# Kernel optimization log

Measured on AMD Instinct MI355X. Metric: run time of the kernel, lower is better.

## Reference

```python
import jax, jax.numpy as jnp
import numpy as np

E = 1024      # embedding_size
K = 64        # key_size
D = 64        # head_size
S = 1024      # context_size
V = 32000     # vocab_size
H = 16        # layer_size (heads per layer)
L = 8         # num_layers
B = 2


def _pe():
    pos = jnp.arange(S, dtype=jnp.float32)[:, None]
    i = jnp.arange(E, dtype=jnp.float32)[None, :]
    ang = pos / jnp.power(10000.0, 2.0 * i / E)
    return jnp.where((jnp.arange(E) % 2 == 0)[None, :], jnp.sin(ang), jnp.cos(ang))


def setup_inputs() -> dict:
    key = jax.random.key(0)
    ks = iter(jax.random.split(key, 32))
    s = 0.02
    n = lambda shape: jax.random.normal(next(ks), shape, dtype=jnp.float32) * s
    inp = {
        "tokens": jax.random.randint(next(ks), (B, S), 0, V),
        "emb": n((V, E)),
        "pe": _pe(),
        "k1w": n((L, H, K, E)), "k1b": n((L, H, K)),
        "k2w": n((L, H, K, K)), "k2b": n((L, H, K)),
        "q1w": n((L, H, K, E)), "q1b": n((L, H, K)),
        "q2w": n((L, H, K, K)), "q2b": n((L, H, K)),
        "vw": n((L, H, D, E)), "vb": n((L, H, D)),
        "lnw": jnp.ones((L, E), jnp.float32), "lnb": jnp.zeros((L, E), jnp.float32),
        "p1w": n((L, E, E)), "p1b": n((L, E)),
        "p2w": n((L, E, E)), "p2b": n((L, E)),
        "predw": n((V, E)), "predb": n((V,)),
    }
    return inp


def reference(tokens, emb, pe, k1w, k1b, k2w, k2b, q1w, q1b, q2w, q2b,
              vw, vb, lnw, lnb, p1w, p1b, p2w, p2b, predw, predb):
    relu = jax.nn.relu
    x = emb[tokens] + pe[:tokens.shape[1]]                       # [B,S,E]
    seq = tokens.shape[1]
    # Faithful to original: tril (past+diag) gets the -1e10 penalty.
    mask = jnp.tril(jnp.ones((seq, seq), x.dtype)) * -1e10
    for l in range(L):
        # two-layer ReLU MLPs for K and Q, batched over heads
        k = relu(jnp.einsum('bse,hke->bhsk', x, k1w[l]) + k1b[l][None, :, None, :])
        k = relu(jnp.einsum('bhsk,hjk->bhsj', k, k2w[l]) + k2b[l][None, :, None, :])
        q = relu(jnp.einsum('bse,hke->bhsk', x, q1w[l]) + q1b[l][None, :, None, :])
        q = relu(jnp.einsum('bhsk,hjk->bhsj', q, q2w[l]) + q2b[l][None, :, None, :])
        v = jnp.einsum('bse,hde->bhsd', x, vw[l]) + vb[l][None, :, None, :]
        scores = jnp.einsum('bhsk,bhtk->bhst', q, k) / (K ** 0.5) + mask
        w = jax.nn.softmax(scores, axis=-1)
        o = jnp.einsum('bhst,bhtd->bhsd', w, v)                  # [B,H,S,D]
        o = o.transpose(0, 2, 1, 3).reshape(x.shape[0], seq, H * D)
        y = x + o
        mu = y.mean(-1, keepdims=True)
        var = ((y - mu) ** 2).mean(-1, keepdims=True)
        yn = (y - mu) / jnp.sqrt(var + 1e-5) * lnw[l] + lnb[l]
        h1 = relu(yn @ p1w[l].T + p1b[l])
        x = relu(h1 @ p2w[l].T + p2b[l])
    logits = x @ predw.T + predb                                 # [B,S,V]
    return logits
```

## Files before the change

### kernel.cpp

```cpp
#include <hip/hip_runtime.h>


typedef __attribute__((ext_vector_type(8))) short bf16x8;
typedef __attribute__((ext_vector_type(4))) float f32x4;

#define L_ 8
#define S_ 1024
#define E_ 1024
#define B_ 2
#define H_ 16
#define V_ 32000
#define M_ 2048

__device__ __forceinline__ unsigned short f2b(float f) {
  union { float f; unsigned int u; } v; v.f = f;
  unsigned int r = v.u + 0x7FFFu + ((v.u >> 16) & 1u);
  return (unsigned short)(r >> 16);
}

#define GLDS16(gptr, lptr)                                                            \
  __builtin_amdgcn_global_load_lds(                                                   \
      (const __attribute__((address_space(1))) unsigned int*)(gptr),                  \
      (__attribute__((address_space(3))) unsigned int*)(lptr), 16, 0, 0)

__global__ void cvt_kernel(const float* __restrict__ src, unsigned short* __restrict__ dst) {
  size_t i = ((size_t)blockIdx.x * 256 + threadIdx.x) * 4;
  float4 v = *(const float4*)(src + i);
  unsigned short* d = dst + i;
  d[0] = f2b(v.x); d[1] = f2b(v.y); d[2] = f2b(v.z); d[3] = f2b(v.w);
}

__global__ void cvt_seg_kernel(const float* __restrict__ src, unsigned short* __restrict__ dst,
                               int perLayer, int dstStride, int dstOff) {
  size_t i = ((size_t)blockIdx.x * 256 + threadIdx.x) * 4;
  int l = (int)(i / perLayer);
  int off = (int)(i - (size_t)l * perLayer);
  float4 v = *(const float4*)(src + i);
  unsigned short* d = dst + (size_t)l * dstStride + dstOff + off;
  d[0] = f2b(v.x); d[1] = f2b(v.y); d[2] = f2b(v.z); d[3] = f2b(v.w);
}

__global__ void biascat_kernel(const float* __restrict__ k1b, const float* __restrict__ q1b,
                               const float* __restrict__ vb, float* __restrict__ bcat) {
  int i = blockIdx.x * 256 + threadIdx.x;
  int l = i / 3072, j = i - l * 3072;
  float v;
  if (j < 1024)      v = k1b[l * 1024 + j];
  else if (j < 2048) v = q1b[l * 1024 + j - 1024];
  else               v = vb [l * 1024 + j - 2048];
  bcat[i] = v;
}

__global__ void embed_kernel(const int* __restrict__ tokens, const float* __restrict__ emb,
                             const float* __restrict__ pe, float* __restrict__ x32,
                             unsigned short* __restrict__ xb) {
  int row = blockIdx.x;
  int s = row & (S_ - 1);
  int e0 = threadIdx.x * 4;
  int tok = tokens[row];
  float4 ev = *(const float4*)(emb + (size_t)tok * E_ + e0);
  float4 pv = *(const float4*)(pe + (size_t)s * E_ + e0);
  float4 v; v.x = ev.x + pv.x; v.y = ev.y + pv.y; v.z = ev.z + pv.z; v.w = ev.w + pv.w;
  *(float4*)(x32 + (size_t)row * E_ + e0) = v;
  ushort4 o; o.x = f2b(v.x); o.y = f2b(v.y); o.z = f2b(v.z); o.w = f2b(v.w);
  *(ushort4*)(xb + (size_t)row * E_ + e0) = o;
}

template <int BM, int BN, int RELU, int OBF, int OF32, int VT>
__global__ __launch_bounds__(256) void gemm97(
    const unsigned short* __restrict__ A, const unsigned short* __restrict__ W,
    const float* __restrict__ bias, unsigned short* __restrict__ Cb,
    float* __restrict__ Cf, unsigned short* __restrict__ vTp,
    int K, int N, int reluN) {
  constexpr int AR = BM / 64;
  constexpr int BR = BN / 64;
  constexpr int FM = BM / 32;
  constexpr int FN = BN / 32;
  __shared__ __align__(16) unsigned short sA[BM * 32];
  __shared__ __align__(16) unsigned short sB[BN * 32];
  const int tid = threadIdx.x;
  const int lane = tid & 63, wave = tid >> 6;
  const int l16 = lane & 15, lhi = lane >> 4;

  const int gx = gridDim.x, nwg = gx * gridDim.y;
  int o = blockIdx.y * gx + blockIdx.x;
  int wg = ((nwg & 7) == 0) ? ((o & 7) * (nwg >> 3) + (o >> 3)) : o;
  const int row0 = (wg % gx) * BM, col0 = (wg / gx) * BN;

  const int wm = (wave >> 1) * (BM / 2), wn = (wave & 1) * (BN / 2);

  const int srow = wave * 16 + (lane >> 2);
  const int scol = ((lane & 3) ^ ((lane >> 3) & 3)) * 8;
  const int cx = (lhi ^ ((l16 >> 1) & 3)) * 8;

  f32x4 acc[FM][FN] = {};

  for (int k0 = 0; k0 < K; k0 += 32) {
#pragma unroll
    for (int r = 0; r < AR; r++)
      GLDS16(A + (size_t)(row0 + r * 64 + srow) * K + k0 + scol,
             sA + r * 2048 + wave * 512);
#pragma unroll
    for (int r = 0; r < BR; r++)
      GLDS16(W + (size_t)(col0 + r * 64 + srow) * K + k0 + scol,
             sB + r * 2048 + wave * 512);
    __syncthreads();

    bf16x8 af[FM], bf[FN];
#pragma unroll
    for (int i = 0; i < FM; i++)
      af[i] = *(const bf16x8*)(sA + (wm + i * 16 + l16) * 32 + cx);
#pragma unroll
    for (int j = 0; j < FN; j++)
      bf[j] = *(const bf16x8*)(sB + (wn + j * 16 + l16) * 32 + cx);
#pragma unroll
    for (int i = 0; i < FM; i++)
#pragma unroll
      for (int j = 0; j < FN; j++)
        acc[i][j] = __builtin_amdgcn_mfma_f32_16x16x32_bf16(bf[j], af[i], acc[i][j], 0, 0, 0);
    __syncthreads();
  }

#pragma unroll
  for (int j = 0; j < FN; j++) {
    const int colb = col0 + wn + j * 16 + lhi * 4;
    const float4 bv = *(const float4*)(bias + colb);
    const bool dorelu = (RELU == 1) || (RELU == 2 && colb < reluN);
#pragma unroll
    for (int i = 0; i < FM; i++) {
      const int row = row0 + wm + i * 16 + l16;
      float v0 = acc[i][j][0] + bv.x, v1 = acc[i][j][1] + bv.y;
      float v2 = acc[i][j][2] + bv.z, v3 = acc[i][j][3] + bv.w;
      if (dorelu) {
        v0 = fmaxf(v0, 0.f); v1 = fmaxf(v1, 0.f);
        v2 = fmaxf(v2, 0.f); v3 = fmaxf(v3, 0.f);
      }
      if (OBF) {
        ushort4 ob; ob.x = f2b(v0); ob.y = f2b(v1); ob.z = f2b(v2); ob.w = f2b(v3);
        *(ushort4*)(Cb + (size_t)row * N + colb) = ob;
      }
      if (OF32) {
        float4 of; of.x = v0; of.y = v1; of.z = v2; of.w = v3;
        *(float4*)(Cf + (size_t)row * N + colb) = of;
      }
      if (VT) {
        if (colb - lhi * 4 >= 2048) {
          const int hd0 = colb - 2048;
          const int bq = row >> 10, s = row & 1023;
          unsigned short* vr = vTp + ((size_t)(bq << 10) + hd0) * 1024 + s;
          vr[0] = f2b(v0); vr[1024] = f2b(v1); vr[2048] = f2b(v2); vr[3072] = f2b(v3);
        }
      }
    }
  }
}

__global__ __launch_bounds__(512, 2) void gemm256(
    const unsigned short* __restrict__ A, const unsigned short* __restrict__ W,
    const float* __restrict__ bias, float* __restrict__ Cf) {
  constexpr int KK = 1024;
  constexpr int NT = 32;
  __shared__ __align__(16) unsigned short sA[3][8192];
  __shared__ __align__(16) unsigned short sB[3][8192];
  const int tid = threadIdx.x;
  const int lane = tid & 63, wave = tid >> 6;
  const int l16 = lane & 15, lhi = lane >> 4;
  const int wr = wave >> 2, wc = wave & 3;

  const int o = blockIdx.x;
  const int wg = (o & 7) * 125 + (o >> 3);
  const int row0 = (wg & 7) * 256;
  const int col0 = (wg >> 3) * 256;

  const int pr0 = tid >> 2;
  const int xc = ((tid & 3) ^ ((pr0 >> 1) & 3)) * 8;
  const int ldsx = (lhi ^ ((l16 >> 1) & 3)) * 8;

  f32x4 acc[8][4] = {};

  auto stage = [&](int kt) {
    const int slot = kt % 3;
    const int k0 = kt * 32;
#pragma unroll
    for (int is = 0; is < 2; is++) {
      GLDS16(A + (size_t)(row0 + is * 128 + pr0) * KK + k0 + xc,
             &sA[slot][(is * 512 + (tid & ~63)) * 8]);
      GLDS16(W + (size_t)(col0 + is * 128 + pr0) * KK + k0 + xc,
             &sB[slot][(is * 512 + (tid & ~63)) * 8]);
    }
  };

  stage(0);
  stage(1);

  for (int kt = 0; kt < NT; kt++) {
    const int slot = kt % 3;
    if (kt == NT - 1) { asm volatile("s_waitcnt vmcnt(0)" ::: "memory"); }
    else              { asm volatile("s_waitcnt vmcnt(4)" ::: "memory"); }
    __builtin_amdgcn_s_barrier();
    __builtin_amdgcn_sched_barrier(0);

    const unsigned short* sa = &sA[slot][(wr * 128) * 32];
    const unsigned short* sb = &sB[slot][(wc * 64) * 32];
    bf16x8 bf[4];
#pragma unroll
    for (int j = 0; j < 4; j++)
      bf[j] = *(const bf16x8*)(sb + (j * 16 + l16) * 32 + ldsx);

#pragma unroll
    for (int ip = 0; ip < 4; ip++) {
      bf16x8 af0 = *(const bf16x8*)(sa + ((ip * 2) * 16 + l16) * 32 + ldsx);
      bf16x8 af1 = *(const bf16x8*)(sa + ((ip * 2 + 1) * 16 + l16) * 32 + ldsx);
      if (ip == 0 && kt + 2 < NT) stage(kt + 2);
      __builtin_amdgcn_s_setprio(1);
#pragma unroll
      for (int j = 0; j < 4; j++)
        acc[ip * 2][j] = __builtin_amdgcn_mfma_f32_16x16x32_bf16(bf[j], af0, acc[ip * 2][j], 0, 0, 0);
#pragma unroll
      for (int j = 0; j < 4; j++)
        acc[ip * 2 + 1][j] = __builtin_amdgcn_mfma_f32_16x16x32_bf16(bf[j], af1, acc[ip * 2 + 1][j], 0, 0, 0);
      __builtin_amdgcn_s_setprio(0);
    }
  }

#pragma unroll
  for (int j = 0; j < 4; j++) {
    const int colb = col0 + wc * 64 + j * 16 + lhi * 4;
    const float4 bv = *(const float4*)(bias + colb);
#pragma unroll
    for (int i = 0; i < 8; i++) {
      const int row = row0 + wr * 128 + i * 16 + l16;
      float4 of;
      of.x = acc[i][j][0] + bv.x; of.y = acc[i][j][1] + bv.y;
      of.z = acc[i][j][2] + bv.z; of.w = acc[i][j][3] + bv.w;
      *(float4*)(Cf + (size_t)row * V_ + colb) = of;
    }
  }
}

__global__ __launch_bounds__(256) void k2q2_kernel(
    const unsigned short* __restrict__ kqv, const unsigned short* __restrict__ wk2,
    const unsigned short* __restrict__ wq2, const float* __restrict__ k2b,
    const float* __restrict__ q2b, unsigned short* __restrict__ kbuf,
    unsigned short* __restrict__ qbuf) {
  const int m0 = blockIdx.x * 64;
  const int h = blockIdx.y;
  const int which = blockIdx.z;
  const unsigned short* Ap = kqv + (which ? 1024 : 0) + h * 64;
  const unsigned short* Wp = (which ? wq2 : wk2) + h * 4096;
  const float* bias = (which ? q2b : k2b) + h * 64;
  unsigned short* out = (which ? qbuf : kbuf) + h * 64;
  const int lane = threadIdx.x & 63, wave = threadIdx.x >> 6;
  const int l16 = lane & 15, lhi = lane >> 4;
  const int mw = m0 + wave * 16;

  f32x4 acc[4] = {};
#pragma unroll
  for (int ks = 0; ks < 2; ks++) {
    bf16x8 a = *(const bf16x8*)(Ap + (size_t)(mw + l16) * 3072 + ks * 32 + (lhi << 3));
#pragma unroll
    for (int j = 0; j < 4; j++) {
      bf16x8 b = *(const bf16x8*)(Wp + (j * 16 + l16) * 64 + ks * 32 + (lhi << 3));
      acc[j] = __builtin_amdgcn_mfma_f32_16x16x32_bf16(a, b, acc[j], 0, 0, 0);
    }
  }
#pragma unroll
  for (int j = 0; j < 4; j++) {
    float bv = bias[j * 16 + l16];
#pragma unroll
    for (int r = 0; r < 4; r++) {
      int row = mw + (lhi << 2) + r;
      float v = fmaxf(acc[j][r] + bv, 0.f);
      out[(size_t)row * 1024 + j * 16 + l16] = f2b(v);
    }
  }
}

__global__ __launch_bounds__(128) void attn_kernel(
    const unsigned short* __restrict__ qbuf,
    const unsigned short* __restrict__ kbuf,
    const unsigned short* __restrict__ vT,
    float* __restrict__ o32) {
  constexpr int LD = 72;
  __shared__ __align__(16) unsigned short sP[2 * 16 * LD];
  const int bid = blockIdx.x;
  const int bh = bid & 31, qt = bid >> 5;
  const int b = bh >> 4, h = bh & 15;
  const int tid = threadIdx.x, lane = tid & 63, w = tid >> 6;
  const int l16 = lane & 15, lhi = lane >> 4;
  const int base = b * S_;
  const int qrow = qt * 32 + w * 16 + l16;

  bf16x8 aq[2];
#pragma unroll
  for (int ks = 0; ks < 2; ks++)
    aq[ks] = *(const bf16x8*)(qbuf + (size_t)(base + qrow) * 1024 + h * 64 + ks * 32 + (lhi << 3));

  f32x4 oacc[4] = {};
  float mrun[4], lrun[4];
#pragma unroll
  for (int r = 0; r < 4; r++) { mrun[r] = -1e10f; lrun[r] = 0.f; }
  const int srow = qt * 32 + w * 16 + (lhi << 2);
  const int t0s = (qt == 31) ? 0 : ((qt >> 1) << 6);

  unsigned short* sPw = sP + w * 16 * LD;

  for (int t0 = t0s; t0 < S_; t0 += 64) {
    f32x4 sacc[4] = {};
#pragma unroll
    for (int ks = 0; ks < 2; ks++) {
#pragma unroll
      for (int nt = 0; nt < 4; nt++) {
        bf16x8 bk = *(const bf16x8*)(kbuf + (size_t)(base + t0 + nt * 16 + l16) * 1024 +
                                     h * 64 + ks * 32 + (lhi << 3));
        sacc[nt] = __builtin_amdgcn_mfma_f32_16x16x32_bf16(aq[ks], bk, sacc[nt], 0, 0, 0);
      }
    }
    float p[4][4];
#pragma unroll
    for (int nt = 0; nt < 4; nt++) {
      int tcol = t0 + nt * 16 + l16;
#pragma unroll
      for (int r = 0; r < 4; r++) {
        float v = sacc[nt][r] * 0.125f;
        if (tcol <= srow + r) v = -1e10f;
        p[nt][r] = v;
      }
    }
#pragma unroll
    for (int r = 0; r < 4; r++) {
      float m = fmaxf(fmaxf(p[0][r], p[1][r]), fmaxf(p[2][r], p[3][r]));
#pragma unroll
      for (int off = 1; off < 16; off <<= 1) m = fmaxf(m, __shfl_xor(m, off, 16));
      float mnew = fmaxf(mrun[r], m);
      float alpha = __expf(mrun[r] - mnew);
      mrun[r] = mnew;
      float rs = 0.f;
#pragma unroll
      for (int nt = 0; nt < 4; nt++) {
        float e = __expf(p[nt][r] - mnew);
        p[nt][r] = e; rs += e;
      }
#pragma unroll
      for (int off = 1; off < 16; off <<= 1) rs += __shfl_xor(rs, off, 16);
      lrun[r] = lrun[r] * alpha + rs;
      oacc[0][r] *= alpha; oacc[1][r] *= alpha; oacc[2][r] *= alpha; oacc[3][r] *= alpha;
    }
#pragma unroll
    for (int nt = 0; nt < 4; nt++)
#pragma unroll
      for (int r = 0; r < 4; r++)
        sPw[((lhi << 2) + r) * LD + nt * 16 + l16] = f2b(p[nt][r]);
#pragma unroll
    for (int ks = 0; ks < 2; ks++) {
      bf16x8 ap = *(const bf16x8*)(sPw + l16 * LD + ks * 32 + (lhi << 3));
#pragma unroll
      for (int nt = 0; nt < 4; nt++) {
        bf16x8 bv = *(const bf16x8*)(vT + (size_t)(bh * 64 + nt * 16 + l16) * 1024 +
                                     t0 + ks * 32 + (lhi << 3));
        oacc[nt] = __builtin_amdgcn_mfma_f32_16x16x32_bf16(ap, bv, oacc[nt], 0, 0, 0);
      }
    }
  }
#pragma unroll
  for (int nt = 0; nt < 4; nt++) {
#pragma unroll
    for (int r = 0; r < 4; r++) {
      int row = srow + r;
      o32[(size_t)(base + row) * 1024 + h * 64 + nt * 16 + l16] = oacc[nt][r] / lrun[r];
    }
  }
}

__global__ __launch_bounds__(256) void ln_kernel(
    const float* __restrict__ x32, const float* __restrict__ o32,
    const float* __restrict__ lnw, const float* __restrict__ lnb,
    unsigned short* __restrict__ yn) {
  __shared__ float red[8];
  const int row = blockIdx.x, tid = threadIdx.x;
  const int lane = tid & 63, wave = tid >> 6;
  const int e0 = tid * 4;
  float4 xv = *(const float4*)(x32 + (size_t)row * E_ + e0);
  float4 ov = *(const float4*)(o32 + (size_t)row * E_ + e0);
  float y0 = xv.x + ov.x, y1 = xv.y + ov.y, y2 = xv.z + ov.z, y3 = xv.w + ov.w;
  float s = y0 + y1 + y2 + y3;
  float sq = y0 * y0 + y1 * y1 + y2 * y2 + y3 * y3;
#pragma unroll
  for (int off = 32; off > 0; off >>= 1) {
    s += __shfl_xor(s, off, 64);
    sq += __shfl_xor(sq, off, 64);
  }
  if (lane == 0) { red[wave * 2] = s; red[wave * 2 + 1] = sq; }
  __syncthreads();
  float ts = red[0] + red[2] + red[4] + red[6];
  float tsq = red[1] + red[3] + red[5] + red[7];
  float mu = ts * (1.f / E_);
  float var = tsq * (1.f / E_) - mu * mu;
  float rstd = rsqrtf(var + 1e-5f);
  float4 gv = *(const float4*)(lnw + e0);
  float4 bv = *(const float4*)(lnb + e0);
  ushort4 o;
  o.x = f2b((y0 - mu) * rstd * gv.x + bv.x);
  o.y = f2b((y1 - mu) * rstd * gv.y + bv.y);
  o.z = f2b((y2 - mu) * rstd * gv.z + bv.z);
  o.w = f2b((y3 - mu) * rstd * gv.w + bv.w);
  *(ushort4*)(yn + (size_t)row * E_ + e0) = o;
}

extern "C" void kernel_launch(void* const* d_in, const int* in_sizes, int n_in,
                              void* d_out, int out_size, void* d_ws, size_t ws_size,
                              hipStream_t stream) {
  const int* tokens  = (const int*)d_in[0];
  const float* emb   = (const float*)d_in[1];
  const float* pe    = (const float*)d_in[2];
  const float* k1w   = (const float*)d_in[3];
  const float* k1b   = (const float*)d_in[4];
  const float* k2w   = (const float*)d_in[5];
  const float* k2b   = (const float*)d_in[6];
  const float* q1w   = (const float*)d_in[7];
  const float* q1b   = (const float*)d_in[8];
  const float* q2w   = (const float*)d_in[9];
  const float* q2b   = (const float*)d_in[10];
  const float* vw    = (const float*)d_in[11];
  const float* vb    = (const float*)d_in[12];
  const float* lnw   = (const float*)d_in[13];
  const float* lnb   = (const float*)d_in[14];
  const float* p1w   = (const float*)d_in[15];
  const float* p1b   = (const float*)d_in[16];
  const float* p2w   = (const float*)d_in[17];
  const float* p2b   = (const float*)d_in[18];
  const float* predw = (const float*)d_in[19];
  const float* predb = (const float*)d_in[20];
  float* out = (float*)d_out;

  char* p = (char*)d_ws;
  auto alloc = [&](size_t bytes) -> char* {
    char* r = p; p += (bytes + 255) & ~(size_t)255; return r;
  };
  unsigned short* wcat  = (unsigned short*)alloc((size_t)L_ * 3072 * 1024 * 2);
  unsigned short* wk2   = (unsigned short*)alloc((size_t)L_ * H_ * 64 * 64 * 2);
  unsigned short* wq2   = (unsigned short*)alloc((size_t)L_ * H_ * 64 * 64 * 2);
  unsigned short* wp1   = (unsigned short*)alloc((size_t)L_ * 1024 * 1024 * 2);
  unsigned short* wp2   = (unsigned short*)alloc((size_t)L_ * 1024 * 1024 * 2);
  unsigned short* wpred = (unsigned short*)alloc((size_t)V_ * 1024 * 2);
  float*          bcat  = (float*)alloc((size_t)L_ * 3072 * 4);
  float*          x32   = (float*)alloc((size_t)M_ * 1024 * 4);
  unsigned short* xb    = (unsigned short*)alloc((size_t)M_ * 1024 * 2);
  unsigned short* kqv   = (unsigned short*)alloc((size_t)M_ * 3072 * 2);
  unsigned short* kbuf  = (unsigned short*)alloc((size_t)M_ * 1024 * 2);
  unsigned short* qbuf  = (unsigned short*)alloc((size_t)M_ * 1024 * 2);
  unsigned short* vTb   = (unsigned short*)alloc((size_t)32 * 64 * 1024 * 2);
  float*          o32   = (float*)alloc((size_t)M_ * 1024 * 4);
  unsigned short* yn    = (unsigned short*)alloc((size_t)M_ * 1024 * 2);
  unsigned short* h1    = (unsigned short*)alloc((size_t)M_ * 1024 * 2);
  if ((size_t)(p - (char*)d_ws) > ws_size) return;

  cvt_seg_kernel<<<8192, 256, 0, stream>>>(k1w, wcat, 1048576, 3145728, 0);
  cvt_seg_kernel<<<8192, 256, 0, stream>>>(q1w, wcat, 1048576, 3145728, 1048576);
  cvt_seg_kernel<<<8192, 256, 0, stream>>>(vw,  wcat, 1048576, 3145728, 2097152);
  cvt_kernel<<<512, 256, 0, stream>>>(k2w, wk2);
  cvt_kernel<<<512, 256, 0, stream>>>(q2w, wq2);
  cvt_kernel<<<8192, 256, 0, stream>>>(p1w, wp1);
  cvt_kernel<<<8192, 256, 0, stream>>>(p2w, wp2);
  cvt_kernel<<<32000, 256, 0, stream>>>(predw, wpred);
  biascat_kernel<<<96, 256, 0, stream>>>(k1b, q1b, vb, bcat);

  embed_kernel<<<M_, 256, 0, stream>>>(tokens, emb, pe, x32, xb);

  for (int l = 0; l < L_; l++) {
    const unsigned short* wcat_l = wcat + (size_t)l * 3072 * 1024;
    const float* bcat_l = bcat + (size_t)l * 3072;
    const unsigned short* wk2_l = wk2 + (size_t)l * H_ * 64 * 64;
    const unsigned short* wq2_l = wq2 + (size_t)l * H_ * 64 * 64;
    const unsigned short* wp1_l = wp1 + (size_t)l * 1024 * 1024;
    const unsigned short* wp2_l = wp2 + (size_t)l * 1024 * 1024;

    gemm97<128, 128, 2, 1, 0, 1><<<dim3(16, 24), 256, 0, stream>>>(
        xb, wcat_l, bcat_l, kqv, nullptr, vTb, 1024, 3072, 2048);
    k2q2_kernel<<<dim3(32, 16, 2), 256, 0, stream>>>(
        kqv, wk2_l, wq2_l, k2b + l * 1024, q2b + l * 1024, kbuf, qbuf);
    attn_kernel<<<1024, 128, 0, stream>>>(qbuf, kbuf, vTb, o32);
    ln_kernel<<<M_, 256, 0, stream>>>(x32, o32, lnw + l * 1024, lnb + l * 1024, yn);
    gemm97<64, 128, 1, 1, 0, 0><<<dim3(32, 8), 256, 0, stream>>>(
        yn, wp1_l, p1b + l * 1024, h1, nullptr, nullptr, 1024, 1024, 0);
    gemm97<64, 128, 1, 1, 1, 0><<<dim3(32, 8), 256, 0, stream>>>(
        h1, wp2_l, p2b + l * 1024, xb, x32, nullptr, 1024, 1024, 0);
  }

  gemm256<<<1000, 512, 0, stream>>>(xb, wpred, predb, out);
}
```

Measured before the change: 1.545 ms.

## Double-buffer K/V register loads in attention and fuse weight conversion launches

The attention inner loop now prefetches the next 64-column K and V tiles into a second register buffer while the MFMAs and softmax run on the current tile, hiding global-load latency. It also merges the eight separate fp32-to-bf16 weight conversion launches into one kernel that dispatches segments by thread index, cutting launch overhead. The prefetch doubles the K/V register footprint, which can raise VGPR pressure and lower occupancy.

```diff
diff --git a/kernel.cpp b/kernel.cpp
--- a/kernel.cpp
+++ b/kernel.cpp
@@ -23,21 +23,30 @@
       (const __attribute__((address_space(1))) unsigned int*)(gptr),                  \
       (__attribute__((address_space(3))) unsigned int*)(lptr), 16, 0, 0)
 
-__global__ void cvt_kernel(const float* __restrict__ src, unsigned short* __restrict__ dst) {
-  size_t i = ((size_t)blockIdx.x * 256 + threadIdx.x) * 4;
-  float4 v = *(const float4*)(src + i);
-  unsigned short* d = dst + i;
-  d[0] = f2b(v.x); d[1] = f2b(v.y); d[2] = f2b(v.z); d[3] = f2b(v.w);
-}
-
-__global__ void cvt_seg_kernel(const float* __restrict__ src, unsigned short* __restrict__ dst,
-                               int perLayer, int dstStride, int dstOff) {
-  size_t i = ((size_t)blockIdx.x * 256 + threadIdx.x) * 4;
-  int l = (int)(i / perLayer);
-  int off = (int)(i - (size_t)l * perLayer);
-  float4 v = *(const float4*)(src + i);
-  unsigned short* d = dst + (size_t)l * dstStride + dstOff + off;
-  d[0] = f2b(v.x); d[1] = f2b(v.y); d[2] = f2b(v.z); d[3] = f2b(v.w);
+__global__ void cvt_all_kernel(
+    const float* __restrict__ k1w, const float* __restrict__ q1w,
+    const float* __restrict__ vw,  const float* __restrict__ k2w,
+    const float* __restrict__ q2w, const float* __restrict__ p1w,
+    const float* __restrict__ p2w, const float* __restrict__ predw,
+    unsigned short* __restrict__ wcat, unsigned short* __restrict__ wk2,
+    unsigned short* __restrict__ wq2,  unsigned short* __restrict__ wp1,
+    unsigned short* __restrict__ wp2,  unsigned short* __restrict__ wpred) {
+  size_t u = (size_t)blockIdx.x * 256 + threadIdx.x;
+  const float* src; unsigned short* dst;
+  if (u < 6291456) {
+    int seg = (int)(u / 2097152);
+    size_t e0 = (u - (size_t)seg * 2097152) * 4;
+    const float* s = (seg == 0) ? k1w : (seg == 1) ? q1w : vw;
+    src = s + e0;
+    int l = (int)(e0 >> 20), off = (int)(e0 & 1048575);
+    dst = wcat + (size_t)l * 3145728 + (size_t)seg * 1048576 + off;
+  } else if (u < 6422528) { size_t e = (u - 6291456) * 4;  src = k2w + e;   dst = wk2 + e; }
+  else if (u < 6553600)   { size_t e = (u - 6422528) * 4;  src = q2w + e;   dst = wq2 + e; }
+  else if (u < 8650752)   { size_t e = (u - 6553600) * 4;  src = p1w + e;   dst = wp1 + e; }
+  else if (u < 10747904)  { size_t e = (u - 8650752) * 4;  src = p2w + e;   dst = wp2 + e; }
+  else                    { size_t e = (u - 10747904) * 4; src = predw + e; dst = wpred + e; }
+  float4 v = *(const float4*)src;
+  dst[0] = f2b(v.x); dst[1] = f2b(v.y); dst[2] = f2b(v.z); dst[3] = f2b(v.w);
 }
 
 __global__ void biascat_kernel(const float* __restrict__ k1b, const float* __restrict__ q1b,
@@ -305,17 +314,28 @@
 
   unsigned short* sPw = sP + w * 16 * LD;
 
-  for (int t0 = t0s; t0 < S_; t0 += 64) {
+  bf16x8 kA[8], vA[8], kB[8], vB[8];
+
+  auto loadKV = [&](int t0, bf16x8* kd, bf16x8* vd) {
+#pragma unroll
+    for (int nt = 0; nt < 4; nt++) {
+#pragma unroll
+      for (int ks = 0; ks < 2; ks++) {
+        kd[nt * 2 + ks] = *(const bf16x8*)(kbuf + (size_t)(base + t0 + nt * 16 + l16) * 1024 +
+                                           h * 64 + ks * 32 + (lhi << 3));
+        vd[nt * 2 + ks] = *(const bf16x8*)(vT + (size_t)(bh * 64 + nt * 16 + l16) * 1024 +
+                                           t0 + ks * 32 + (lhi << 3));
+      }
+    }
+  };
+
+  auto compute = [&](int t0, const bf16x8* kc, const bf16x8* vc) {
     f32x4 sacc[4] = {};
 #pragma unroll
-    for (int ks = 0; ks < 2; ks++) {
-#pragma unroll
-      for (int nt = 0; nt < 4; nt++) {
-        bf16x8 bk = *(const bf16x8*)(kbuf + (size_t)(base + t0 + nt * 16 + l16) * 1024 +
-                                     h * 64 + ks * 32 + (lhi << 3));
-        sacc[nt] = __builtin_amdgcn_mfma_f32_16x16x32_bf16(aq[ks], bk, sacc[nt], 0, 0, 0);
-      }
-    }
+    for (int ks = 0; ks < 2; ks++)
+#pragma unroll
+      for (int nt = 0; nt < 4; nt++)
+        sacc[nt] = __builtin_amdgcn_mfma_f32_16x16x32_bf16(aq[ks], kc[nt * 2 + ks], sacc[nt], 0, 0, 0);
     float p[4][4];
 #pragma unroll
     for (int nt = 0; nt < 4; nt++) {
@@ -355,13 +375,22 @@
     for (int ks = 0; ks < 2; ks++) {
       bf16x8 ap = *(const bf16x8*)(sPw + l16 * LD + ks * 32 + (lhi << 3));
 #pragma unroll
-      for (int nt = 0; nt < 4; nt++) {
-        bf16x8 bv = *(const bf16x8*)(vT + (size_t)(bh * 64 + nt * 16 + l16) * 1024 +
-                                     t0 + ks * 32 + (lhi << 3));
-        oacc[nt] = __builtin_amdgcn_mfma_f32_16x16x32_bf16(ap, bv, oacc[nt], 0, 0, 0);
-      }
-    }
-  }
+      for (int nt = 0; nt < 4; nt++)
+        oacc[nt] = __builtin_amdgcn_mfma_f32_16x16x32_bf16(ap, vc[nt * 2 + ks], oacc[nt], 0, 0, 0);
+    }
+  };
+
+  loadKV(t0s, kA, vA);
+  int t0 = t0s;
+  while (true) {
+    if (t0 + 64 < S_) loadKV(t0 + 64, kB, vB);
+    compute(t0, kA, vA);
+    t0 += 64; if (t0 >= S_) break;
+    if (t0 + 64 < S_) loadKV(t0 + 64, kA, vA);
+    compute(t0, kB, vB);
+    t0 += 64; if (t0 >= S_) break;
+  }
+
 #pragma unroll
   for (int nt = 0; nt < 4; nt++) {
 #pragma unroll
@@ -455,14 +484,8 @@
   unsigned short* h1    = (unsigned short*)alloc((size_t)M_ * 1024 * 2);
   if ((size_t)(p - (char*)d_ws) > ws_size) return;
 
-  cvt_seg_kernel<<<8192, 256, 0, stream>>>(k1w, wcat, 1048576, 3145728, 0);
-  cvt_seg_kernel<<<8192, 256, 0, stream>>>(q1w, wcat, 1048576, 3145728, 1048576);
-  cvt_seg_kernel<<<8192, 256, 0, stream>>>(vw,  wcat, 1048576, 3145728, 2097152);
-  cvt_kernel<<<512, 256, 0, stream>>>(k2w, wk2);
-  cvt_kernel<<<512, 256, 0, stream>>>(q2w, wq2);
-  cvt_kernel<<<8192, 256, 0, stream>>>(p1w, wp1);
-  cvt_kernel<<<8192, 256, 0, stream>>>(p2w, wp2);
-  cvt_kernel<<<32000, 256, 0, stream>>>(predw, wpred);
+  cvt_all_kernel<<<73984, 256, 0, stream>>>(k1w, q1w, vw, k2w, q2w, p1w, p2w, predw,
+                                            wcat, wk2, wq2, wp1, wp2, wpred);
   biascat_kernel<<<96, 256, 0, stream>>>(k1b, q1b, vb, bcat);
 
   embed_kernel<<<M_, 256, 0, stream>>>(tokens, emb, pe, x32, xb);
```

Result: faster. 1.505 ms (-2.6%).
